# Optimization experiments

Hardware: AMD Instinct MI355X
Metric: run time of the kernel (lower is better)

Reference implementation:

```python
import jax, jax.numpy as jnp
import numpy as np

TOP_K = 2
SCALING = 32.0 / 16.0  # lora_alpha / r

N, D, O = 4096, 4096, 4096   # tokens, in_features, out_features
E, H, R_RANK = 8, 3, 16      # experts, B-heads per expert, lora rank
W_SCALE = 0.02               # keep logits in a sane range


def setup_inputs() -> dict:
    key = jax.random.key(0)
    ks = jax.random.split(key, 6)
    return {
        "x": jax.random.normal(ks[0], (N, D), jnp.float32),
        "base_W": jax.random.normal(ks[1], (D, O), jnp.float32) * W_SCALE,
        "router_W": jax.random.normal(ks[2], (E, D), jnp.float32) * W_SCALE,
        "A": jax.random.normal(ks[3], (E, D, R_RANK), jnp.float32) * W_SCALE,
        "B": jax.random.normal(ks[4], (E, H, R_RANK, O), jnp.float32) * W_SCALE,
        "R": jax.random.normal(ks[5], (E, D, H), jnp.float32) * W_SCALE,
    }


def reference(x, base_W, router_W, A, B, R):
    # Base dense layer
    base = x @ base_W                                   # [N, O]
    # Expert router: softmax over experts, top-k gate renormalized
    probs = jax.nn.softmax(x @ router_W.T, axis=-1)     # [N, E]
    topv, topi = jax.lax.top_k(probs, TOP_K)            # [N, k]
    topv = topv / topv.sum(-1, keepdims=True)
    n_idx = jnp.arange(x.shape[0])[:, None]
    gate = jnp.zeros_like(probs).at[n_idx, topi].set(topv)  # dense [N, E] gate, 0 off top-k
    # Shared lora_A per expert
    a = jnp.einsum('nd,edr->ner', x, A)                 # [N, E, r]
    # Per-expert head router over lora_B heads
    head_w = jax.nn.softmax(jnp.einsum('nd,edh->neh', x, R), axis=-1)  # [N, E, H]
    # Head-weighted B projections, combined with expert gates
    delta = jnp.einsum('ner,neh,ehro,ne->no', a, head_w, B, gate)      # [N, O]
    return base + SCALING * delta
```

## Files before the change

kernel.cpp:

```cpp
#include <hip/hip_runtime.h>
#include <hip/hip_bf16.h>
#include <math.h>

typedef __bf16 bf16_t;
typedef __bf16 bf16x4_t __attribute__((ext_vector_type(4)));
typedef __bf16 bf16x8_t __attribute__((ext_vector_type(8)));
typedef float  f32x4_t  __attribute__((ext_vector_type(4)));

#define N_TOK 4096
#define D_IN  4096
#define O_OUT 4096
#define NEXP  8
#define NHEAD 3
#define RANK  16
#define KC2   384
#define PCOLS 256
#define NKZ   8
#define SCALING_F 2.0f


__device__ __forceinline__ void transpose_tile(const float* __restrict__ src,
                                               bf16_t* __restrict__ dst,
                                               int Rr, int Cc, int r0, int c0,
                                               float (*tile)[65]) {
  int q  = threadIdx.x & 15;
  int r4 = threadIdx.x >> 4;
  #pragma unroll
  for (int g = 0; g < 4; ++g) {
    int r = r4 + g * 16;
    float4 v = *(const float4*)(src + (size_t)(r0 + r) * Cc + c0 + q * 4);
    tile[r][q * 4 + 0] = v.x; tile[r][q * 4 + 1] = v.y;
    tile[r][q * 4 + 2] = v.z; tile[r][q * 4 + 3] = v.w;
  }
  __syncthreads();
  int j  = threadIdx.x & 7;
  int cc = threadIdx.x >> 3;
  #pragma unroll
  for (int h = 0; h < 2; ++h) {
    int c = cc + h * 32;
    bf16x8_t o;
    #pragma unroll
    for (int i = 0; i < 8; ++i) o[i] = (bf16_t)tile[j * 8 + i][c];
    *(bf16x8_t*)(dst + (size_t)(c0 + c) * Rr + r0 + j * 8) = o;
  }
}

__global__ __launch_bounds__(256) void prep_kernel(const float* __restrict__ x,
                                                   const float* __restrict__ base_W,
                                                   const float* __restrict__ rw,
                                                   const float* __restrict__ A,
                                                   const float* __restrict__ B,
                                                   const float* __restrict__ Rm,
                                                   bf16_t* __restrict__ xb,
                                                   bf16_t* __restrict__ WbT,
                                                   bf16_t* __restrict__ BbT,
                                                   bf16_t* __restrict__ PabT,
                                                   int* __restrict__ gidx,
                                                   float* __restrict__ gwv) {
  __shared__ float tile[64][65];
  int b = blockIdx.x;
  if (b < 4096) {
    transpose_tile(base_W, WbT, 4096, 4096, (b & 63) * 64, (b >> 6) * 64, tile);
  } else if (b < 5120) {
    int lane = threadIdx.x & 63;
    int wv = threadIdx.x >> 6;
    int n = (b - 4096) * 4 + wv;
    const float4* xv = (const float4*)(x + (size_t)n * D_IN);
    bf16x4_t* xo = (bf16x4_t*)(xb + (size_t)n * D_IN);
    float acc[NEXP] = {0, 0, 0, 0, 0, 0, 0, 0};
    for (int d = lane; d < D_IN / 4; d += 64) {
      float4 xx = xv[d];
      bf16x4_t ob = { (bf16_t)xx.x, (bf16_t)xx.y, (bf16_t)xx.z, (bf16_t)xx.w };
      xo[d] = ob;
      #pragma unroll
      for (int e = 0; e < NEXP; ++e) {
        float4 ww = ((const float4*)(rw + (size_t)e * D_IN))[d];
        acc[e] += xx.x * ww.x + xx.y * ww.y + xx.z * ww.z + xx.w * ww.w;
      }
    }
    #pragma unroll
    for (int e = 0; e < NEXP; ++e) {
      float v = acc[e];
      #pragma unroll
      for (int o = 32; o > 0; o >>= 1) v += __shfl_down(v, o);
      acc[e] = v;
    }
    if (lane == 0) {
      int i0 = 0; float l0 = acc[0];
      #pragma unroll
      for (int e = 1; e < NEXP; ++e) if (acc[e] > l0) { l0 = acc[e]; i0 = e; }
      int i1 = -1; float l1 = -3.4e38f;
      #pragma unroll
      for (int e = 0; e < NEXP; ++e) if (e != i0 && acc[e] > l1) { l1 = acc[e]; i1 = e; }
      float w0 = 1.f / (1.f + expf(l1 - l0));
      gidx[2 * n] = i0; gidx[2 * n + 1] = i1;
      gwv[2 * n] = w0;  gwv[2 * n + 1] = 1.f - w0;
    }
  } else if (b < 5504) {
    int t = b - 5120;
    transpose_tile(B, BbT, KC2, 4096, (t % 6) * 64, (t / 6) * 64, tile);
  } else {
    int c = b - 5504;
    for (int d = threadIdx.x; d < D_IN; d += 256) {
      float v = 0.f;
      if (c < 128) {
        int e = c >> 4, r = c & 15;
        v = A[((size_t)e * D_IN + d) * RANK + r];
      } else if (c < 152) {
        int qq = c - 128; int e = qq / 3, h = qq - 3 * e;
        v = Rm[((size_t)e * D_IN + d) * NHEAD + h];
      }
      PabT[(size_t)c * D_IN + d] = (bf16_t)v;
    }
  }
}

__global__ void gating_kernel(const float* __restrict__ projP, const int* __restrict__ gidx,
                              const float* __restrict__ gwv, bf16_t* __restrict__ C2b) {
  int n = blockIdx.x;
  int c = threadIdx.x;
  int e = c / 48;
  int h = (c % 48) / 16;
  int r = c & 15;
  int i0 = gidx[2 * n], i1 = gidx[2 * n + 1];
  float g = (e == i0) ? gwv[2 * n] : (e == i1) ? gwv[2 * n + 1] : 0.f;
  float val = 0.f;
  if (g != 0.f) {
    const float* p0 = projP + (size_t)n * PCOLS;
    const size_t S = (size_t)N_TOK * PCOLS;
    float h0 = 0.f, h1 = 0.f, h2 = 0.f, av = 0.f;
    #pragma unroll
    for (int z = 0; z < NKZ; ++z) {
      const float* pz = p0 + (size_t)z * S;
      h0 += pz[128 + e * 3 + 0];
      h1 += pz[128 + e * 3 + 1];
      h2 += pz[128 + e * 3 + 2];
      av += pz[e * 16 + r];
    }
    float mx = fmaxf(h0, fmaxf(h1, h2));
    float e0 = expf(h0 - mx), e1 = expf(h1 - mx), e2 = expf(h2 - mx);
    float hw = (h == 0 ? e0 : h == 1 ? e1 : e2) / (e0 + e1 + e2);
    val = SCALING_F * g * hw * av;
  }
  C2b[(size_t)n * KC2 + c] = (bf16_t)val;
}

__device__ __forceinline__ void run_kloop(f32x4_t (&acc)[4][4], bf16_t* sA, bf16_t* sB,
                                          const bf16_t* __restrict__ Ab, int lda,
                                          const bf16_t* __restrict__ Bb, int ldb, int K) {
  const int tid = threadIdx.x;
  const int lane = tid & 63;
  const int w = tid >> 6;
  const int wm = (w >> 1) * 64;
  const int wn = (w & 1) * 64;
  const int qd = lane >> 4;
  const int ln = lane & 15;
  const int sw = ln & 7;

  size_t offA[4], offB[4];
  int lo[4];
  #pragma unroll
  for (int t = 0; t < 4; ++t) {
    int c = tid + t * 256;
    int m = c >> 3, kc = (c & 7) ^ (m & 7);
    offA[t] = (size_t)m * lda + kc * 8;
    offB[t] = (size_t)m * ldb + kc * 8;
    lo[t] = c * 8;
  }
  int rowA[4], rowB[4];
  #pragma unroll
  for (int i = 0; i < 4; ++i) {
    rowA[i] = (wm + i * 16 + ln) * 64;
    rowB[i] = (wn + i * 16 + ln) * 64;
  }

  for (int k0 = 0; k0 < K; k0 += 64) {
    __syncthreads();
    #pragma unroll
    for (int t = 0; t < 4; ++t)
      __builtin_amdgcn_global_load_lds(
          (const __attribute__((address_space(1))) void*)(Ab + k0 + offA[t]),
          (__attribute__((address_space(3))) void*)(sA + lo[t]), 16, 0, 0);
    #pragma unroll
    for (int t = 0; t < 4; ++t)
      __builtin_amdgcn_global_load_lds(
          (const __attribute__((address_space(1))) void*)(Bb + k0 + offB[t]),
          (__attribute__((address_space(3))) void*)(sB + lo[t]), 16, 0, 0);
    __syncthreads();
    #pragma unroll
    for (int s = 0; s < 2; ++s) {
      bf16x8_t af[4], bfr[4];
      int kx = ((s * 4 + qd) ^ sw) * 8;
      #pragma unroll
      for (int i = 0; i < 4; ++i) af[i]  = *(const bf16x8_t*)(sA + rowA[i] + kx);
      #pragma unroll
      for (int i = 0; i < 4; ++i) bfr[i] = *(const bf16x8_t*)(sB + rowB[i] + kx);
      #pragma unroll
      for (int i = 0; i < 4; ++i)
        #pragma unroll
        for (int j = 0; j < 4; ++j)
          acc[i][j] = __builtin_amdgcn_mfma_f32_16x16x32_bf16(af[i], bfr[j], acc[i][j], 0, 0, 0);
    }
  }
}

__global__ __launch_bounds__(256) void gemm_proj_kernel(const bf16_t* __restrict__ xb,
                                                        const bf16_t* __restrict__ PabT,
                                                        float* __restrict__ projP) {
  __shared__ bf16_t sA[128 * 64];
  __shared__ bf16_t sB[128 * 64];
  int bm = blockIdx.x, bn = blockIdx.y, kz = blockIdx.z;
  f32x4_t acc[4][4] = {};
  run_kloop(acc, sA, sB,
            xb + (size_t)bm * 128 * D_IN + kz * 512, D_IN,
            PabT + (size_t)bn * 128 * D_IN + kz * 512, D_IN, 512);
  const int lane = threadIdx.x & 63, w = threadIdx.x >> 6;
  const int wm = (w >> 1) * 64, wn = (w & 1) * 64, qd = lane >> 4, ln = lane & 15;
  float* Cb = projP + (size_t)kz * N_TOK * PCOLS + (size_t)bm * 128 * PCOLS + bn * 128;
  #pragma unroll
  for (int i = 0; i < 4; ++i)
    #pragma unroll
    for (int j = 0; j < 4; ++j) {
      int col = wn + j * 16 + ln;
      #pragma unroll
      for (int rg = 0; rg < 4; ++rg) {
        int row = wm + i * 16 + qd * 4 + rg;
        Cb[(size_t)row * PCOLS + col] = acc[i][j][rg];
      }
    }
}


__device__ __forceinline__ void stage2(const bf16_t* __restrict__ G, int k0,
                                       bf16_t* lbase, size_t g0, size_t g1, int tid) {
  __builtin_amdgcn_global_load_lds(
      (const __attribute__((address_space(1))) void*)(G + g0 + k0),
      (__attribute__((address_space(3))) void*)(lbase + tid * 8), 16, 0, 0);
  __builtin_amdgcn_global_load_lds(
      (const __attribute__((address_space(1))) void*)(G + g1 + k0),
      (__attribute__((address_space(3))) void*)(lbase + 4096 + tid * 8), 16, 0, 0);
}

template <int N>
__device__ __forceinline__ void vm_wait() {
  if constexpr (N == 8)      asm volatile("s_waitcnt vmcnt(8)" ::: "memory");
  else if constexpr (N == 4) asm volatile("s_waitcnt vmcnt(4)" ::: "memory");
  else if constexpr (N == 0) asm volatile("s_waitcnt vmcnt(0)" ::: "memory");
}

template <int MB>
__device__ __forceinline__ void mfma16(f32x4_t (&acc)[8][4], const bf16x8_t (&af)[4],
                                       const bf16x8_t (&bv)[4]) {
  __builtin_amdgcn_s_setprio(1);
  #pragma unroll
  for (int mi = 0; mi < 4; ++mi)
    #pragma unroll
    for (int nj = 0; nj < 4; ++nj)
      acc[MB + mi][nj] =
          __builtin_amdgcn_mfma_f32_16x16x32_bf16(af[mi], bv[nj], acc[MB + mi][nj], 0, 0, 0);
  __builtin_amdgcn_s_setprio(0);
}

template <int SC, bool STAGE, int VMN, bool NEXTRD>
__device__ __forceinline__ void tbodyP(f32x4_t (&acc)[8][4], bf16_t* sring,
                                       const bf16_t* __restrict__ Ag,
                                       const bf16_t* __restrict__ Bg, int k3,
                                       size_t gA0, size_t gA1, size_t gB0, size_t gB1,
                                       int aoff, int boff, int tid,
                                       bf16x8_t (&bv)[4], bf16x8_t (&a0)[4]) {
  constexpr int SS = (SC + 3) & 3;
  constexpr int SN = (SC + 1) & 3;
  if constexpr (STAGE) {
    stage2(Ag, k3, sring + SS * 16384, gA0, gA1, tid);
    stage2(Bg, k3, sring + SS * 16384 + 8192, gB0, gB1, tid);
  }
  const bf16_t* pA = sring + SC * 16384 + aoff;
  bf16x8_t a1[4];
  mfma16<0>(acc, a0, bv);
  #pragma unroll
  for (int mi = 0; mi < 4; ++mi) a1[mi] = *(const bf16x8_t*)(pA + (4 + mi) * 512);
  vm_wait<VMN>();
  __builtin_amdgcn_s_barrier();
  mfma16<4>(acc, a1, bv);
  if constexpr (NEXTRD) {
    const bf16_t* qA = sring + SN * 16384 + aoff;
    const bf16_t* qB = sring + SN * 16384 + 8192 + boff;
    #pragma unroll
    for (int nj = 0; nj < 4; ++nj) bv[nj] = *(const bf16x8_t*)(qB + nj * 512);
    #pragma unroll
    for (int mi = 0; mi < 4; ++mi) a0[mi] = *(const bf16x8_t*)(qA + mi * 512);
  }
  __builtin_amdgcn_sched_barrier(0);
  __builtin_amdgcn_s_barrier();
}

template <int K>
__device__ __forceinline__ void kloopP(f32x4_t (&acc)[8][4], bf16_t* sring,
                                       const bf16_t* __restrict__ A, int lda,
                                       const bf16_t* __restrict__ B, int ldb,
                                       int tid, int aoff, int boff) {
  constexpr int T = K / 32;
  static_assert((T & 3) == 0, "T must be multiple of 4");
  const int s0 = tid,       r0 = s0 >> 2, c0 = (s0 & 3) ^ ((r0 >> 1) & 3);
  const int s1 = 512 + tid, r1 = s1 >> 2, c1 = (s1 & 3) ^ ((r1 >> 1) & 3);
  const size_t gA0 = (size_t)r0 * lda + c0 * 8, gA1 = (size_t)r1 * lda + c1 * 8;
  const size_t gB0 = (size_t)r0 * ldb + c0 * 8, gB1 = (size_t)r1 * ldb + c1 * 8;

  #pragma unroll
  for (int t = 0; t < 3; ++t) {
    stage2(A, t * 32, sring + t * 16384, gA0, gA1, tid);
    stage2(B, t * 32, sring + t * 16384 + 8192, gB0, gB1, tid);
  }
  asm volatile("s_waitcnt vmcnt(8)" ::: "memory");
  __builtin_amdgcn_s_barrier();
  bf16x8_t bv[4], a0[4];
  {
    const bf16_t* qA = sring + aoff;
    const bf16_t* qB = sring + 8192 + boff;
    #pragma unroll
    for (int nj = 0; nj < 4; ++nj) bv[nj] = *(const bf16x8_t*)(qB + nj * 512);
    #pragma unroll
    for (int mi = 0; mi < 4; ++mi) a0[mi] = *(const bf16x8_t*)(qA + mi * 512);
  }
  constexpr int TM = T - 3;
  int t = 0;
  for (; t + 3 < TM; t += 4) {
    tbodyP<0,true,8,true>(acc, sring, A, B, (t+3)*32, gA0,gA1,gB0,gB1, aoff,boff,tid, bv,a0);
    tbodyP<1,true,8,true>(acc, sring, A, B, (t+4)*32, gA0,gA1,gB0,gB1, aoff,boff,tid, bv,a0);
    tbodyP<2,true,8,true>(acc, sring, A, B, (t+5)*32, gA0,gA1,gB0,gB1, aoff,boff,tid, bv,a0);
    tbodyP<3,true,8,true>(acc, sring, A, B, (t+6)*32, gA0,gA1,gB0,gB1, aoff,boff,tid, bv,a0);
  }
  tbodyP<0,true,8,true>(acc, sring, A, B, (t+3)*32, gA0,gA1,gB0,gB1, aoff,boff,tid, bv,a0);
  tbodyP<1,false,4,true >(acc, sring, A, B, 0, gA0,gA1,gB0,gB1, aoff,boff,tid, bv,a0);
  tbodyP<2,false,0,true >(acc, sring, A, B, 0, gA0,gA1,gB0,gB1, aoff,boff,tid, bv,a0);
  tbodyP<3,false,-1,false>(acc, sring, A, B, 0, gA0,gA1,gB0,gB1, aoff,boff,tid, bv,a0);
}

__global__ __launch_bounds__(512, 1) void gemm_fused256(const bf16_t* __restrict__ xb,
                                                        const bf16_t* __restrict__ WbT,
                                                        const bf16_t* __restrict__ C2b,
                                                        const bf16_t* __restrict__ BbT,
                                                        float* __restrict__ out) {
  __shared__ __align__(16) bf16_t sring[4 * 16384];
  const int tid = threadIdx.x;
  const int lane = tid & 63;
  const int w = tid >> 6;
  const int wm = w >> 2;
  const int wn = w & 3;
  const int qd = lane >> 4;
  const int ln = lane & 15;
  const int swz8 = ((qd ^ ((ln >> 1) & 3)) << 3);

  int b = blockIdx.x;
  int sw = (b & 7) * 32 + (b >> 3);
  int bm = sw >> 4, bn = sw & 15;

  const int aoff = (wm * 128 + ln) * 32 + swz8;
  const int boff = (wn * 64 + ln) * 32 + swz8;

  f32x4_t acc[8][4] = {};

  kloopP<D_IN>(acc, sring, xb  + (size_t)bm * 256 * D_IN, D_IN,
                           WbT + (size_t)bn * 256 * D_IN, D_IN, tid, aoff, boff);
  kloopP<KC2>(acc, sring, C2b + (size_t)bm * 256 * KC2,  KC2,
                          BbT + (size_t)bn * 256 * KC2,  KC2,  tid, aoff, boff);

  float* Cb = out + (size_t)(bm * 256 + wm * 128) * O_OUT + bn * 256 + wn * 64;
  #pragma unroll
  for (int mi = 0; mi < 8; ++mi)
    #pragma unroll
    for (int nj = 0; nj < 4; ++nj)
      #pragma unroll
      for (int rg = 0; rg < 4; ++rg)
        Cb[(size_t)(mi * 16 + qd * 4 + rg) * O_OUT + nj * 16 + ln] = acc[mi][nj][rg];
}

extern "C" void kernel_launch(void* const* d_in, const int* in_sizes, int n_in,
                              void* d_out, int out_size, void* d_ws, size_t ws_size,
                              hipStream_t stream) {
  const float* x       = (const float*)d_in[0];
  const float* base_W  = (const float*)d_in[1];
  const float* routerW = (const float*)d_in[2];
  const float* A       = (const float*)d_in[3];
  const float* B       = (const float*)d_in[4];
  const float* Rm      = (const float*)d_in[5];
  float* out = (float*)d_out;
  char* ws = (char*)d_ws;

  bf16_t* xb   = (bf16_t*)(ws);
  bf16_t* WbT  = (bf16_t*)(ws + 33554432);
  bf16_t* PabT = (bf16_t*)(ws + 67108864);
  bf16_t* BbT  = (bf16_t*)(ws + 69206016);
  bf16_t* C2b  = (bf16_t*)(ws + 72351744);
  int*    gidx = (int*)   (ws + 75497472);
  float*  gwv  = (float*) (ws + 75530240);
  float*  projP = out;

  prep_kernel<<<5760, 256, 0, stream>>>(x, base_W, routerW, A, B, Rm,
                                        xb, WbT, BbT, PabT, gidx, gwv);
  gemm_proj_kernel<<<dim3(32, 2, NKZ), 256, 0, stream>>>(xb, PabT, projP);
  gating_kernel<<<4096, 384, 0, stream>>>(projP, gidx, gwv, C2b);
  gemm_fused256<<<dim3(256), 512, 0, stream>>>(xb, WbT, C2b, BbT, out);
}
```

Before: 358.5 us.

## Use 16 waves per block with smaller per-wave tiles in fused GEMM

Result: no change. 360.5 us (+0.6%).

```diff
diff --git a/kernel.cpp b/kernel.cpp
--- a/kernel.cpp
+++ b/kernel.cpp
@@ -231,116 +231,86 @@
 }
 
 
-__device__ __forceinline__ void stage2(const bf16_t* __restrict__ G, int k0,
-                                       bf16_t* lbase, size_t g0, size_t g1, int tid) {
+__device__ __forceinline__ void stage1(const bf16_t* __restrict__ G, int k0,
+                                       bf16_t* lbase, size_t g, int tid) {
   __builtin_amdgcn_global_load_lds(
-      (const __attribute__((address_space(1))) void*)(G + g0 + k0),
+      (const __attribute__((address_space(1))) void*)(G + g + k0),
       (__attribute__((address_space(3))) void*)(lbase + tid * 8), 16, 0, 0);
-  __builtin_amdgcn_global_load_lds(
-      (const __attribute__((address_space(1))) void*)(G + g1 + k0),
-      (__attribute__((address_space(3))) void*)(lbase + 4096 + tid * 8), 16, 0, 0);
 }
 
 template <int N>
 __device__ __forceinline__ void vm_wait() {
-  if constexpr (N == 8)      asm volatile("s_waitcnt vmcnt(8)" ::: "memory");
+  if constexpr (N == 6)      asm volatile("s_waitcnt vmcnt(6)" ::: "memory");
   else if constexpr (N == 4) asm volatile("s_waitcnt vmcnt(4)" ::: "memory");
+  else if constexpr (N == 2) asm volatile("s_waitcnt vmcnt(2)" ::: "memory");
   else if constexpr (N == 0) asm volatile("s_waitcnt vmcnt(0)" ::: "memory");
 }
 
-template <int MB>
-__device__ __forceinline__ void mfma16(f32x4_t (&acc)[8][4], const bf16x8_t (&af)[4],
-                                       const bf16x8_t (&bv)[4]) {
-  __builtin_amdgcn_s_setprio(1);
-  #pragma unroll
-  for (int mi = 0; mi < 4; ++mi)
-    #pragma unroll
-    for (int nj = 0; nj < 4; ++nj)
-      acc[MB + mi][nj] =
-          __builtin_amdgcn_mfma_f32_16x16x32_bf16(af[mi], bv[nj], acc[MB + mi][nj], 0, 0, 0);
-  __builtin_amdgcn_s_setprio(0);
-}
-
-template <int SC, bool STAGE, int VMN, bool NEXTRD>
-__device__ __forceinline__ void tbodyP(f32x4_t (&acc)[8][4], bf16_t* sring,
+template <int SC, bool STAGE, int VMN>
+__device__ __forceinline__ void tbodyS(f32x4_t (&acc)[4][4], bf16_t* sring,
                                        const bf16_t* __restrict__ Ag,
                                        const bf16_t* __restrict__ Bg, int k3,
-                                       size_t gA0, size_t gA1, size_t gB0, size_t gB1,
-                                       int aoff, int boff, int tid,
-                                       bf16x8_t (&bv)[4], bf16x8_t (&a0)[4]) {
+                                       size_t gA, size_t gB, int aoff, int boff, int tid) {
   constexpr int SS = (SC + 3) & 3;
-  constexpr int SN = (SC + 1) & 3;
   if constexpr (STAGE) {
-    stage2(Ag, k3, sring + SS * 16384, gA0, gA1, tid);
-    stage2(Bg, k3, sring + SS * 16384 + 8192, gB0, gB1, tid);
-  }
-  const bf16_t* pA = sring + SC * 16384 + aoff;
-  bf16x8_t a1[4];
-  mfma16<0>(acc, a0, bv);
-  #pragma unroll
-  for (int mi = 0; mi < 4; ++mi) a1[mi] = *(const bf16x8_t*)(pA + (4 + mi) * 512);
+    stage1(Ag, k3, sring + SS * 16384, gA, tid);
+    stage1(Bg, k3, sring + SS * 16384 + 8192, gB, tid);
+  }
   vm_wait<VMN>();
   __builtin_amdgcn_s_barrier();
-  mfma16<4>(acc, a1, bv);
-  if constexpr (NEXTRD) {
-    const bf16_t* qA = sring + SN * 16384 + aoff;
-    const bf16_t* qB = sring + SN * 16384 + 8192 + boff;
-    #pragma unroll
-    for (int nj = 0; nj < 4; ++nj) bv[nj] = *(const bf16x8_t*)(qB + nj * 512);
-    #pragma unroll
-    for (int mi = 0; mi < 4; ++mi) a0[mi] = *(const bf16x8_t*)(qA + mi * 512);
-  }
+  const bf16_t* pA = sring + SC * 16384 + aoff;
+  const bf16_t* pB = sring + SC * 16384 + 8192 + boff;
+  bf16x8_t af[4], bv[4];
+  #pragma unroll
+  for (int nj = 0; nj < 4; ++nj) bv[nj] = *(const bf16x8_t*)(pB + nj * 512);
+  #pragma unroll
+  for (int mi = 0; mi < 4; ++mi) af[mi] = *(const bf16x8_t*)(pA + mi * 512);
+  __builtin_amdgcn_s_setprio(1);
+  #pragma unroll
+  for (int mi = 0; mi < 4; ++mi)
+    #pragma unroll
+    for (int nj = 0; nj < 4; ++nj)
+      acc[mi][nj] = __builtin_amdgcn_mfma_f32_16x16x32_bf16(af[mi], bv[nj], acc[mi][nj], 0, 0, 0);
+  __builtin_amdgcn_s_setprio(0);
   __builtin_amdgcn_sched_barrier(0);
   __builtin_amdgcn_s_barrier();
 }
 
 template <int K>
-__device__ __forceinline__ void kloopP(f32x4_t (&acc)[8][4], bf16_t* sring,
+__device__ __forceinline__ void kloopS(f32x4_t (&acc)[4][4], bf16_t* sring,
                                        const bf16_t* __restrict__ A, int lda,
                                        const bf16_t* __restrict__ B, int ldb,
                                        int tid, int aoff, int boff) {
   constexpr int T = K / 32;
   static_assert((T & 3) == 0, "T must be multiple of 4");
-  const int s0 = tid,       r0 = s0 >> 2, c0 = (s0 & 3) ^ ((r0 >> 1) & 3);
-  const int s1 = 512 + tid, r1 = s1 >> 2, c1 = (s1 & 3) ^ ((r1 >> 1) & 3);
-  const size_t gA0 = (size_t)r0 * lda + c0 * 8, gA1 = (size_t)r1 * lda + c1 * 8;
-  const size_t gB0 = (size_t)r0 * ldb + c0 * 8, gB1 = (size_t)r1 * ldb + c1 * 8;
+  const int s = tid, r = s >> 2, c = (s & 3) ^ ((r >> 1) & 3);
+  const size_t gA = (size_t)r * lda + c * 8;
+  const size_t gB = (size_t)r * ldb + c * 8;
 
   #pragma unroll
   for (int t = 0; t < 3; ++t) {
-    stage2(A, t * 32, sring + t * 16384, gA0, gA1, tid);
-    stage2(B, t * 32, sring + t * 16384 + 8192, gB0, gB1, tid);
-  }
-  asm volatile("s_waitcnt vmcnt(8)" ::: "memory");
-  __builtin_amdgcn_s_barrier();
-  bf16x8_t bv[4], a0[4];
-  {
-    const bf16_t* qA = sring + aoff;
-    const bf16_t* qB = sring + 8192 + boff;
-    #pragma unroll
-    for (int nj = 0; nj < 4; ++nj) bv[nj] = *(const bf16x8_t*)(qB + nj * 512);
-    #pragma unroll
-    for (int mi = 0; mi < 4; ++mi) a0[mi] = *(const bf16x8_t*)(qA + mi * 512);
+    stage1(A, t * 32, sring + t * 16384, gA, tid);
+    stage1(B, t * 32, sring + t * 16384 + 8192, gB, tid);
   }
   constexpr int TM = T - 3;
   int t = 0;
   for (; t + 3 < TM; t += 4) {
-    tbodyP<0,true,8,true>(acc, sring, A, B, (t+3)*32, gA0,gA1,gB0,gB1, aoff,boff,tid, bv,a0);
-    tbodyP<1,true,8,true>(acc, sring, A, B, (t+4)*32, gA0,gA1,gB0,gB1, aoff,boff,tid, bv,a0);
-    tbodyP<2,true,8,true>(acc, sring, A, B, (t+5)*32, gA0,gA1,gB0,gB1, aoff,boff,tid, bv,a0);
-    tbodyP<3,true,8,true>(acc, sring, A, B, (t+6)*32, gA0,gA1,gB0,gB1, aoff,boff,tid, bv,a0);
-  }
-  tbodyP<0,true,8,true>(acc, sring, A, B, (t+3)*32, gA0,gA1,gB0,gB1, aoff,boff,tid, bv,a0);
-  tbodyP<1,false,4,true >(acc, sring, A, B, 0, gA0,gA1,gB0,gB1, aoff,boff,tid, bv,a0);
-  tbodyP<2,false,0,true >(acc, sring, A, B, 0, gA0,gA1,gB0,gB1, aoff,boff,tid, bv,a0);
-  tbodyP<3,false,-1,false>(acc, sring, A, B, 0, gA0,gA1,gB0,gB1, aoff,boff,tid, bv,a0);
-}
-
-__global__ __launch_bounds__(512, 1) void gemm_fused256(const bf16_t* __restrict__ xb,
-                                                        const bf16_t* __restrict__ WbT,
-                                                        const bf16_t* __restrict__ C2b,
-                                                        const bf16_t* __restrict__ BbT,
-                                                        float* __restrict__ out) {
+    tbodyS<0,true,6>(acc, sring, A, B, (t+3)*32, gA, gB, aoff, boff, tid);
+    tbodyS<1,true,6>(acc, sring, A, B, (t+4)*32, gA, gB, aoff, boff, tid);
+    tbodyS<2,true,6>(acc, sring, A, B, (t+5)*32, gA, gB, aoff, boff, tid);
+    tbodyS<3,true,6>(acc, sring, A, B, (t+6)*32, gA, gB, aoff, boff, tid);
+  }
+  tbodyS<0,true,6>(acc, sring, A, B, (t+3)*32, gA, gB, aoff, boff, tid);
+  tbodyS<1,false,4>(acc, sring, A, B, 0, gA, gB, aoff, boff, tid);
+  tbodyS<2,false,2>(acc, sring, A, B, 0, gA, gB, aoff, boff, tid);
+  tbodyS<3,false,0>(acc, sring, A, B, 0, gA, gB, aoff, boff, tid);
+}
+
+__global__ __launch_bounds__(1024, 1) void gemm_fused256(const bf16_t* __restrict__ xb,
+                                                         const bf16_t* __restrict__ WbT,
+                                                         const bf16_t* __restrict__ C2b,
+                                                         const bf16_t* __restrict__ BbT,
+                                                         float* __restrict__ out) {
   __shared__ __align__(16) bf16_t sring[4 * 16384];
   const int tid = threadIdx.x;
   const int lane = tid & 63;
@@ -355,19 +325,19 @@
   int sw = (b & 7) * 32 + (b >> 3);
   int bm = sw >> 4, bn = sw & 15;
 
-  const int aoff = (wm * 128 + ln) * 32 + swz8;
+  const int aoff = (wm * 64 + ln) * 32 + swz8;
   const int boff = (wn * 64 + ln) * 32 + swz8;
 
-  f32x4_t acc[8][4] = {};
-
-  kloopP<D_IN>(acc, sring, xb  + (size_t)bm * 256 * D_IN, D_IN,
+  f32x4_t acc[4][4] = {};
+
+  kloopS<D_IN>(acc, sring, xb  + (size_t)bm * 256 * D_IN, D_IN,
                            WbT + (size_t)bn * 256 * D_IN, D_IN, tid, aoff, boff);
-  kloopP<KC2>(acc, sring, C2b + (size_t)bm * 256 * KC2,  KC2,
+  kloopS<KC2>(acc, sring, C2b + (size_t)bm * 256 * KC2,  KC2,
                           BbT + (size_t)bn * 256 * KC2,  KC2,  tid, aoff, boff);
 
-  float* Cb = out + (size_t)(bm * 256 + wm * 128) * O_OUT + bn * 256 + wn * 64;
-  #pragma unroll
-  for (int mi = 0; mi < 8; ++mi)
+  float* Cb = out + (size_t)(bm * 256 + wm * 64) * O_OUT + bn * 256 + wn * 64;
+  #pragma unroll
+  for (int mi = 0; mi < 4; ++mi)
     #pragma unroll
     for (int nj = 0; nj < 4; ++nj)
       #pragma unroll
@@ -400,5 +370,5 @@
                                         xb, WbT, BbT, PabT, gidx, gwv);
   gemm_proj_kernel<<<dim3(32, 2, NKZ), 256, 0, stream>>>(xb, PabT, projP);
   gating_kernel<<<4096, 384, 0, stream>>>(projP, gidx, gwv, C2b);
-  gemm_fused256<<<dim3(256), 512, 0, stream>>>(xb, WbT, C2b, BbT, out);
-}
+  gemm_fused256<<<dim3(256), 1024, 0, stream>>>(xb, WbT, C2b, BbT, out);
+}
```
